# Kernel tuning notes

Measured on AMD Instinct MI355X. Metric: run time of the kernel, lower is better.

The kernel has to match this reference:

```python
import jax, jax.numpy as jnp
import numpy as np

D_MODEL = 1024
NUM_HEAD = 16
D_HEAD = 64


def setup_inputs() -> dict:
    key = jax.random.key(0)
    ks = jax.random.split(key, 9)
    b, p = 8, 1024
    s = 1.0 / np.sqrt(D_MODEL)
    inp = {
        "x": jax.random.normal(ks[0], (b, p, D_MODEL), jnp.float32),
        "w_q": jax.random.uniform(ks[1], (D_MODEL, D_MODEL), jnp.float32, -s, s),
        "b_q": jax.random.uniform(ks[2], (D_MODEL,), jnp.float32, -s, s),
        "w_k": jax.random.uniform(ks[3], (D_MODEL, D_MODEL), jnp.float32, -s, s),
        "b_k": jax.random.uniform(ks[4], (D_MODEL,), jnp.float32, -s, s),
        "w_v": jax.random.uniform(ks[5], (D_MODEL, D_MODEL), jnp.float32, -s, s),
        "b_v": jax.random.uniform(ks[6], (D_MODEL,), jnp.float32, -s, s),
        "w_o": jax.random.uniform(ks[7], (D_MODEL, D_MODEL), jnp.float32, -s, s),
        "b_o": jax.random.uniform(ks[8], (D_MODEL,), jnp.float32, -s, s),
    }
    return inp


def reference(x, w_q, b_q, w_k, b_k, w_v, b_v, w_o, b_o):
    b, p, _ = x.shape
    # projections (torch Linear: y = x @ W.T + b; here weights stored [in,out])
    q = x @ w_q + b_q
    k = x @ w_k + b_k
    v = x @ w_v + b_v
    # [b, h, p, d]
    q = q.reshape(b, p, NUM_HEAD, D_HEAD).transpose(0, 2, 1, 3)
    k = k.reshape(b, p, NUM_HEAD, D_HEAD).transpose(0, 2, 1, 3)
    v = v.reshape(b, p, NUM_HEAD, D_HEAD).transpose(0, 2, 1, 3)
    scale = 1.0 / np.sqrt(D_HEAD).astype(np.float32)
    scores = jnp.einsum("bhqd,bhkd->bhqk", q, k) * scale
    attn = jax.nn.softmax(scores, axis=-1)
    out = jnp.einsum("bhqk,bhkd->bhqd", attn, v)
    out = out.transpose(0, 2, 1, 3).reshape(b, p, D_MODEL)
    return out @ w_o + b_o
```

## Files before the change

### kernel.cpp

```cpp
#include <hip/hip_runtime.h>
#include <stdint.h>


typedef __attribute__((ext_vector_type(8))) short short8;
typedef __attribute__((ext_vector_type(4))) short s16x4;
typedef __attribute__((ext_vector_type(4))) float f32x4;

__device__ __forceinline__ short f2bf(float f) {
  unsigned u = __builtin_bit_cast(unsigned, f);
  u += 0x7fffu + ((u >> 16) & 1u);
  return (short)(u >> 16);
}

__device__ __forceinline__ unsigned pk2bf(float a, float b) {
  unsigned ua = __builtin_bit_cast(unsigned, a);
  unsigned ub = __builtin_bit_cast(unsigned, b);
  ua += 0x7fffu + ((ua >> 16) & 1u);
  ub += 0x7fffu + ((ub >> 16) & 1u);
  return (ua >> 16) | (ub & 0xffff0000u);
}

typedef __attribute__((address_space(3))) void lds_void;
typedef __attribute__((address_space(1))) void gbl_void;
#define GLD16(gp, lp) \
  __builtin_amdgcn_global_load_lds((gbl_void*)(gp), (lds_void*)(lp), 16, 0, 0)

#define MFMA(a, b, c) __builtin_amdgcn_mfma_f32_16x16x32_bf16((a), (b), (c), 0, 0, 0)

__global__ __launch_bounds__(256) void k_prep(const float* __restrict__ x,
                                              short* __restrict__ xb,
                                              const float* __restrict__ s0,
                                              const float* __restrict__ s1,
                                              const float* __restrict__ s2,
                                              const float* __restrict__ s3,
                                              short* __restrict__ d0,
                                              short* __restrict__ d1,
                                              short* __restrict__ d2,
                                              short* __restrict__ d3) {
  if (blockIdx.z == 4) {
    int t = threadIdx.y * 32 + threadIdx.x;
    int bid = blockIdx.y * 32 + blockIdx.x;
#pragma unroll
    for (int j = 0; j < 4; ++j) {
      int i = (bid * 1024 + j * 256 + t) * 8;
      const float4* s = (const float4*)(x + i);
      float4 f0 = s[0], f1 = s[1];
      short8 o;
      o[0] = f2bf(f0.x); o[1] = f2bf(f0.y); o[2] = f2bf(f0.z); o[3] = f2bf(f0.w);
      o[4] = f2bf(f1.x); o[5] = f2bf(f1.y); o[6] = f2bf(f1.z); o[7] = f2bf(f1.w);
      *(short8*)(xb + i) = o;
    }
    return;
  }
  __shared__ float tile[32][33];
  const float* srcs[4] = {s0, s1, s2, s3};
  short* dsts[4] = {d0, d1, d2, d3};
  const float* src = srcs[blockIdx.z];
  short* dst = dsts[blockIdx.z];
  int tx = threadIdx.x, ty = threadIdx.y;
  int x0 = blockIdx.x * 32, y0 = blockIdx.y * 32;
#pragma unroll
  for (int i = 0; i < 32; i += 8)
    tile[ty + i][tx] = src[(y0 + ty + i) * 1024 + x0 + tx];
  __syncthreads();
#pragma unroll
  for (int i = 0; i < 32; i += 8)
    dst[(x0 + ty + i) * 1024 + y0 + tx] = f2bf(tile[tx][ty + i]);
}

template <int MODE>
__global__ __launch_bounds__(256, 3) void k_gemm(const short* __restrict__ A,
                                                 const short* __restrict__ Bt,
                                                 const float* __restrict__ bias0,
                                                 const float* __restrict__ bias1,
                                                 const float* __restrict__ bias2,
                                                 short* __restrict__ o0,
                                                 short* __restrict__ o1,
                                                 short* __restrict__ o2,
                                                 float* __restrict__ of) {
  __shared__ __align__(16) short a_lds[128 * 64];
  __shared__ __align__(16) short b_lds[128 * 64];
  const int tid = threadIdx.x;
  const int l = blockIdx.x;
  const int m0 = ((((l & 7) << 3) | ((l >> 3) & 7))) << 7;
  const int n0 = (l >> 6) << 7;
  const int w = tid >> 6;
  const int lane = tid & 63;
  const int ll = lane & 15;
  const int qd = lane >> 4;
  const int wm = (w & 1) * 64;
  const int wn = (w >> 1) * 64;

  const int srow = tid >> 3;
  const int schunk = ((tid & 7) ^ (srow & 7)) * 8;
  const short* ag = A + (long)(m0 + srow) * 1024 + schunk;
  const short* bg = Bt + (long)(n0 + srow) * 1024 + schunk;

  f32x4 acc[4][4] = {};

  for (int kt = 0; kt < 1024; kt += 64) {
#pragma unroll
    for (int j = 0; j < 4; ++j) {
      GLD16(ag + j * 32768 + kt, &a_lds[j * 2048 + tid * 8]);
      GLD16(bg + j * 32768 + kt, &b_lds[j * 2048 + tid * 8]);
    }
    __syncthreads();
#pragma unroll
    for (int kh = 0; kh < 2; ++kh) {
      const int xoff = (((kh * 4 + qd) ^ (ll & 7)) * 8);
      short8 af[4], bfr[4];
#pragma unroll
      for (int mt = 0; mt < 4; ++mt)
        af[mt] = *(const short8*)&a_lds[(wm + mt * 16 + ll) * 64 + xoff];
#pragma unroll
      for (int nt = 0; nt < 4; ++nt)
        bfr[nt] = *(const short8*)&b_lds[(wn + nt * 16 + ll) * 64 + xoff];
#pragma unroll
      for (int mt = 0; mt < 4; ++mt)
#pragma unroll
        for (int nt = 0; nt < 4; ++nt)
          acc[mt][nt] = MFMA(af[mt], bfr[nt], acc[mt][nt]);
    }
    __syncthreads();
  }

  if (MODE == 0) {
#pragma unroll
    for (int nt = 0; nt < 4; ++nt) {
      int n = n0 + wn + nt * 16 + ll;
      int which = n >> 10;
      int nl = n & 1023;
      int h = nl >> 6, d = n & 63;
      if (which == 2) {
        float bv = bias2[nl];
        const int b = m0 >> 10;
        const int p0 = (m0 & 1023) + wm;
#pragma unroll
        for (int mt = 0; mt < 4; ++mt) {
          int p = p0 + mt * 16 + qd * 4;
          int2 pk;
          pk.x = (int)pk2bf(acc[mt][nt][0] + bv, acc[mt][nt][1] + bv);
          pk.y = (int)pk2bf(acc[mt][nt][2] + bv, acc[mt][nt][3] + bv);
          *(int2*)&o2[(long)(b * 16 + h) * 65536 + d * 1024 + p] = pk;
        }
      } else {
        float bv = (which == 0) ? bias0[nl] : bias1[nl];
        float sc = (which == 0) ? 0.125f : 1.0f;
        short* o = (which == 0) ? o0 : o1;
#pragma unroll
        for (int mt = 0; mt < 4; ++mt) {
#pragma unroll
          for (int r = 0; r < 4; ++r) {
            int m = m0 + wm + mt * 16 + qd * 4 + r;
            int b = m >> 10, p = m & 1023;
            o[(long)(b * 16 + h) * 65536 + p * 64 + d] = f2bf((acc[mt][nt][r] + bv) * sc);
          }
        }
      }
    }
  } else {
#pragma unroll
    for (int nt = 0; nt < 4; ++nt) {
      int n = n0 + wn + nt * 16 + ll;
      float bv = bias0[n];
#pragma unroll
      for (int mt = 0; mt < 4; ++mt) {
#pragma unroll
        for (int r = 0; r < 4; ++r) {
          int m = m0 + wm + mt * 16 + qd * 4 + r;
          of[(long)m * 1024 + n] = acc[mt][nt][r] + bv;
        }
      }
    }
  }
}

__global__ __launch_bounds__(256, 4) void k_attn(const short* __restrict__ Q,
                                                 const short* __restrict__ K,
                                                 const short* __restrict__ VT,
                                                 short* __restrict__ O) {
  __shared__ __align__(16) short k_lds[4096];
  __shared__ __align__(16) short vt_lds[4096];
  __shared__ __align__(16) short p_lds[4][32 * 72];
  const int tid = threadIdx.x;
  const int w = tid >> 6, lane = tid & 63, ll = lane & 15, qd = lane >> 4;
  const int bh = blockIdx.y, qb = blockIdx.x;
  const long hoff = (long)bh * 65536;
  const int qr0 = qb * 128 + w * 32;

  const short* qg = Q + hoff + (long)(qr0 + ll) * 64 + qd * 8;
  short8 qf[2][2];
  qf[0][0] = *(const short8*)qg;
  qf[0][1] = *(const short8*)(qg + 32);
  qf[1][0] = *(const short8*)(qg + 1024);
  qf[1][1] = *(const short8*)(qg + 1024 + 32);

  const int sr = tid >> 3;
  const int swz = (tid & 7) ^ (sr & 7);
  const short* kg = K + hoff + sr * 64 + swz * 8;
  const short* vg = VT + hoff + (long)sr * 1024 + swz * 8;
  short* kl0 = &k_lds[tid * 8];
  short* kl1 = &k_lds[2048 + tid * 8];
  short* vl0 = &vt_lds[tid * 8];
  short* vl1 = &vt_lds[2048 + tid * 8];

  const int swzr = ll & 7;
  const int fro0 = ll * 64 + ((qd ^ swzr) * 8);
  const int fro1 = ll * 64 + (((4 + qd) ^ swzr) * 8);
  short* pw = &p_lds[w][0];

  f32x4 oacc[2][4] = {};
  float l_part[2] = {0.f, 0.f};

  for (int c = 0; c < 16; ++c) {
    GLD16(kg + c * 4096, kl0);
    GLD16(kg + c * 4096 + 2048, kl1);
    GLD16(vg + c * 64, vl0);
    GLD16(vg + c * 64 + 32768, vl1);
    __syncthreads();

    f32x4 s[2][4];
#pragma unroll
    for (int jt = 0; jt < 4; ++jt) {
      short8 kf0 = *(const short8*)&k_lds[jt * 1024 + fro0];
      short8 kf1 = *(const short8*)&k_lds[jt * 1024 + fro1];
      f32x4 t0 = {};
      t0 = MFMA(kf0, qf[0][0], t0);
      t0 = MFMA(kf1, qf[0][1], t0);
      s[0][jt] = t0;
      f32x4 t1 = {};
      t1 = MFMA(kf0, qf[1][0], t1);
      t1 = MFMA(kf1, qf[1][1], t1);
      s[1][jt] = t1;
    }

    short8 pf[2][2];
#pragma unroll
    for (int g = 0; g < 2; ++g) {
      float rs = 0.f;
#pragma unroll
      for (int jt = 0; jt < 4; ++jt)
#pragma unroll
        for (int r = 0; r < 4; ++r) {
          float e = __expf(s[g][jt][r]);
          s[g][jt][r] = e;
          rs += e;
        }
      l_part[g] += rs;
      short* pg = pw + (g * 16 + ll) * 72;
#pragma unroll
      for (int jt = 0; jt < 4; ++jt) {
        int2 pk;
        pk.x = (int)pk2bf(s[g][jt][0], s[g][jt][1]);
        pk.y = (int)pk2bf(s[g][jt][2], s[g][jt][3]);
        *(int2*)&pg[jt * 16 + qd * 4] = pk;
      }
      pf[g][0] = *(const short8*)&pg[qd * 8];
      pf[g][1] = *(const short8*)&pg[32 + qd * 8];
    }

#pragma unroll
    for (int dt = 0; dt < 4; ++dt) {
      short8 vf0 = *(const short8*)&vt_lds[dt * 1024 + fro0];
      short8 vf1 = *(const short8*)&vt_lds[dt * 1024 + fro1];
      oacc[0][dt] = MFMA(vf0, pf[0][0], oacc[0][dt]);
      oacc[0][dt] = MFMA(vf1, pf[0][1], oacc[0][dt]);
      oacc[1][dt] = MFMA(vf0, pf[1][0], oacc[1][dt]);
      oacc[1][dt] = MFMA(vf1, pf[1][1], oacc[1][dt]);
    }
    __syncthreads();
  }

  const int b = bh >> 4, h = bh & 15;
#pragma unroll
  for (int g = 0; g < 2; ++g) {
    float l = l_part[g];
    l += __shfl_xor(l, 16, 64);
    l += __shfl_xor(l, 32, 64);
    const float inv = 1.0f / l;
    const long row = (long)(b * 1024 + qr0 + g * 16 + ll);
#pragma unroll
    for (int dt = 0; dt < 4; ++dt) {
      int2 ov;
      ov.x = (int)pk2bf(oacc[g][dt][0] * inv, oacc[g][dt][1] * inv);
      ov.y = (int)pk2bf(oacc[g][dt][2] * inv, oacc[g][dt][3] * inv);
      *(int2*)&O[row * 1024 + h * 64 + dt * 16 + qd * 4] = ov;
    }
  }
}

extern "C" void kernel_launch(void* const* d_in, const int* in_sizes, int n_in,
                              void* d_out, int out_size, void* d_ws, size_t ws_size,
                              hipStream_t stream) {
  const float* x   = (const float*)d_in[0];
  const float* w_q = (const float*)d_in[1];
  const float* b_q = (const float*)d_in[2];
  const float* w_k = (const float*)d_in[3];
  const float* b_k = (const float*)d_in[4];
  const float* w_v = (const float*)d_in[5];
  const float* b_v = (const float*)d_in[6];
  const float* w_o = (const float*)d_in[7];
  const float* b_o = (const float*)d_in[8];

  char* ws = (char*)d_ws;
  short* xb    = (short*)(ws);
  short* wqkvT = (short*)(ws + (16ull << 20));
  short* woT   = (short*)(ws + (22ull << 20));
  short* qw    = (short*)(ws + (24ull << 20));
  short* kw    = (short*)(ws + (40ull << 20));
  short* vw    = (short*)(ws + (56ull << 20));

  k_prep<<<dim3(32, 32, 5), dim3(32, 8), 0, stream>>>(
      x, xb, w_q, w_k, w_v, w_o,
      wqkvT, wqkvT + (1 << 20), wqkvT + (2 << 20), woT);

  k_gemm<0><<<1536, 256, 0, stream>>>(xb, wqkvT, b_q, b_k, b_v,
                                      qw, kw, vw, nullptr);

  k_attn<<<dim3(8, 128), 256, 0, stream>>>(qw, kw, vw, xb);

  k_gemm<1><<<512, 256, 0, stream>>>(xb, woT, b_o, nullptr, nullptr,
                                     nullptr, nullptr, nullptr, (float*)d_out);
}
```

Baseline: 239.6 us.

## Double-buffer K/V tiles in attention kernel and swap grid axes

The attention kernel now keeps two LDS buffers for K and V^T. It prefetches chunk c+1 with async global-to-LDS loads while chunk c is computed, which is meant to hide global load latency behind the MFMA and softmax work. The per-wave P scratch shrinks to a single 16-row buffer reused for both row groups. The grid swaps its axes, so neighbouring blocks now cover different heads rather than query blocks of the same head, which changes L2 reuse of K/V. Occupancy is lowered from 4 to 3 blocks per CU to make room for the larger LDS footprint.

Result: no change. 239.8 us (+0.1%).

```diff
diff --git a/kernel.cpp b/kernel.cpp
--- a/kernel.cpp
+++ b/kernel.cpp
@@ -175,16 +175,16 @@
   }
 }
 
-__global__ __launch_bounds__(256, 4) void k_attn(const short* __restrict__ Q,
+__global__ __launch_bounds__(256, 3) void k_attn(const short* __restrict__ Q,
                                                  const short* __restrict__ K,
                                                  const short* __restrict__ VT,
                                                  short* __restrict__ O) {
-  __shared__ __align__(16) short k_lds[4096];
-  __shared__ __align__(16) short vt_lds[4096];
-  __shared__ __align__(16) short p_lds[4][32 * 72];
+  __shared__ __align__(16) short k_lds[2][4096];
+  __shared__ __align__(16) short vt_lds[2][4096];
+  __shared__ __align__(16) short p_lds[4][1152];
   const int tid = threadIdx.x;
   const int w = tid >> 6, lane = tid & 63, ll = lane & 15, qd = lane >> 4;
-  const int bh = blockIdx.y, qb = blockIdx.x;
+  const int bh = blockIdx.x, qb = blockIdx.y;
   const long hoff = (long)bh * 65536;
   const int qr0 = qb * 128 + w * 32;
 
@@ -199,10 +199,8 @@
   const int swz = (tid & 7) ^ (sr & 7);
   const short* kg = K + hoff + sr * 64 + swz * 8;
   const short* vg = VT + hoff + (long)sr * 1024 + swz * 8;
-  short* kl0 = &k_lds[tid * 8];
-  short* kl1 = &k_lds[2048 + tid * 8];
-  short* vl0 = &vt_lds[tid * 8];
-  short* vl1 = &vt_lds[2048 + tid * 8];
+  const int sl0 = tid * 8;
+  const int sl1 = 2048 + tid * 8;
 
   const int swzr = ll & 7;
   const int fro0 = ll * 64 + ((qd ^ swzr) * 8);
@@ -212,18 +210,26 @@
   f32x4 oacc[2][4] = {};
   float l_part[2] = {0.f, 0.f};
 
+  GLD16(kg, &k_lds[0][sl0]);
+  GLD16(kg + 2048, &k_lds[0][sl1]);
+  GLD16(vg, &vt_lds[0][sl0]);
+  GLD16(vg + 32768, &vt_lds[0][sl1]);
+  __syncthreads();
+
   for (int c = 0; c < 16; ++c) {
-    GLD16(kg + c * 4096, kl0);
-    GLD16(kg + c * 4096 + 2048, kl1);
-    GLD16(vg + c * 64, vl0);
-    GLD16(vg + c * 64 + 32768, vl1);
-    __syncthreads();
+    const int cur = c & 1, nxt = cur ^ 1;
+    if (c < 15) {
+      GLD16(kg + (c + 1) * 4096, &k_lds[nxt][sl0]);
+      GLD16(kg + (c + 1) * 4096 + 2048, &k_lds[nxt][sl1]);
+      GLD16(vg + (c + 1) * 64, &vt_lds[nxt][sl0]);
+      GLD16(vg + (c + 1) * 64 + 32768, &vt_lds[nxt][sl1]);
+    }
 
     f32x4 s[2][4];
 #pragma unroll
     for (int jt = 0; jt < 4; ++jt) {
-      short8 kf0 = *(const short8*)&k_lds[jt * 1024 + fro0];
-      short8 kf1 = *(const short8*)&k_lds[jt * 1024 + fro1];
+      short8 kf0 = *(const short8*)&k_lds[cur][jt * 1024 + fro0];
+      short8 kf1 = *(const short8*)&k_lds[cur][jt * 1024 + fro1];
       f32x4 t0 = {};
       t0 = MFMA(kf0, qf[0][0], t0);
       t0 = MFMA(kf1, qf[0][1], t0);
@@ -247,22 +253,21 @@
           rs += e;
         }
       l_part[g] += rs;
-      short* pg = pw + (g * 16 + ll) * 72;
 #pragma unroll
       for (int jt = 0; jt < 4; ++jt) {
         int2 pk;
         pk.x = (int)pk2bf(s[g][jt][0], s[g][jt][1]);
         pk.y = (int)pk2bf(s[g][jt][2], s[g][jt][3]);
-        *(int2*)&pg[jt * 16 + qd * 4] = pk;
+        *(int2*)&pw[ll * 72 + jt * 16 + qd * 4] = pk;
       }
-      pf[g][0] = *(const short8*)&pg[qd * 8];
-      pf[g][1] = *(const short8*)&pg[32 + qd * 8];
+      pf[g][0] = *(const short8*)&pw[ll * 72 + qd * 8];
+      pf[g][1] = *(const short8*)&pw[ll * 72 + 32 + qd * 8];
     }
 
 #pragma unroll
     for (int dt = 0; dt < 4; ++dt) {
-      short8 vf0 = *(const short8*)&vt_lds[dt * 1024 + fro0];
-      short8 vf1 = *(const short8*)&vt_lds[dt * 1024 + fro1];
+      short8 vf0 = *(const short8*)&vt_lds[cur][dt * 1024 + fro0];
+      short8 vf1 = *(const short8*)&vt_lds[cur][dt * 1024 + fro1];
       oacc[0][dt] = MFMA(vf0, pf[0][0], oacc[0][dt]);
       oacc[0][dt] = MFMA(vf1, pf[0][1], oacc[0][dt]);
       oacc[1][dt] = MFMA(vf0, pf[1][0], oacc[1][dt]);
@@ -317,7 +322,7 @@
   k_gemm<0><<<1536, 256, 0, stream>>>(xb, wqkvT, b_q, b_k, b_v,
                                       qw, kw, vw, nullptr);
 
-  k_attn<<<dim3(8, 128), 256, 0, stream>>>(qw, kw, vw, xb);
+  k_attn<<<dim3(128, 8), 256, 0, stream>>>(qw, kw, vw, xb);
 
   k_gemm<1><<<512, 256, 0, stream>>>(xb, woT, b_o, nullptr, nullptr,
                                      nullptr, nullptr, nullptr, (float*)d_out);
```
